# Kernel tuning notes

Measured on AMD Instinct MI355X. Metric: run time of the kernel, lower is better.

## Reference

```python
import jax, jax.numpy as jnp
import numpy as np

N, F, E = 100000, 128, 600000
EPS = 1e-5

def setup_inputs() -> dict:
    key = jax.random.key(0)
    ks = jax.random.split(key, 12)
    d = {
        'feature': jax.random.normal(ks[0], (N, F), jnp.float32),
        'edge_index': jax.random.randint(ks[1], (2, E), 0, N, jnp.int64 if jax.config.jax_enable_x64 else jnp.int32).astype(jnp.int32),
        'edge_weight': jax.random.uniform(ks[2], (E,), jnp.float32),
        'Ws': jax.random.normal(ks[3], (F, F), jnp.float32) * (2.0 / F) ** 0.5,
        'bs': jnp.zeros((F,), jnp.float32),
        'Wi': jax.random.normal(ks[4], (F, F), jnp.float32) * (2.0 / F) ** 0.5,
        'bi': jnp.zeros((F,), jnp.float32),
        'Wr': jax.random.normal(ks[5], (F, F), jnp.float32) * (2.0 / F) ** 0.5,
        'br': jnp.zeros((F,), jnp.float32),
        'gamma': jnp.ones((F,), jnp.float32),
        'beta': jnp.zeros((F,), jnp.float32),
        'WtoI': jax.random.normal(ks[6], (2 * F, F), jnp.float32) * (1.0 / (2 * F)) ** 0.5,
        'btoI': jnp.zeros((F,), jnp.float32),
        'WtoR': jax.random.normal(ks[7], (F, F), jnp.float32) * (1.0 / F) ** 0.5,
        'btoR': jnp.zeros((F,), jnp.float32),
        'Wout': jax.random.normal(ks[8], (3 * F, 3), jnp.float32) * (2.0 / (3 * F)) ** 0.5,
        'bout': jnp.zeros((3,), jnp.float32),
    }
    return d

def _bn(x, gamma, beta):
    # BatchNorm1d in training mode: batch mean, biased variance
    m = x.mean(axis=0)
    v = x.var(axis=0)
    return gamma * (x - m) * jax.lax.rsqrt(v + EPS) + beta

def reference(feature, edge_index, edge_weight, Ws, bs, Wi, bi, Wr, br,
              gamma, beta, WtoI, btoI, WtoR, btoR, Wout, bout):
    n = feature.shape[0]
    s = jax.nn.relu(_bn(feature @ Ws + bs + feature, gamma, beta))
    i = jax.nn.relu(_bn(feature @ Wi + bi + feature, gamma, beta))
    r = jax.nn.relu(_bn(feature @ Wr + br + feature, gamma, beta))
    # message passing: gather i at source nodes, weight, scatter-add to dest
    src, dst = edge_index[0], edge_index[1]
    msg = i[src] * edge_weight[:, None]                      # [E, F]
    neighbor_i = jax.ops.segment_sum(msg, dst, num_segments=n)  # [N, F]
    toI = jnp.concatenate([s, neighbor_i], axis=1) @ WtoI + btoI
    toR = i @ WtoR + btoR
    s1 = s - toI
    i1 = i + toI - toR
    r1 = toR + r
    logits = jnp.concatenate([s1, i1, r1], axis=-1) @ Wout + bout  # [N, 3]
    return jax.nn.softmax(logits, axis=-1)
```

## Files before the change

kernel.cpp:

```cpp
#include <hip/hip_runtime.h>
#include <math.h>

#define NFEAT 128
#define EPSBN 1e-5f
#define LDA 136
#define NREP 8

typedef __attribute__((ext_vector_type(8))) short short8;
typedef __attribute__((ext_vector_type(4))) float f32x4;

__device__ __forceinline__ unsigned short f2bf(float x) {
  union { float f; unsigned u; } v; v.f = x;
  unsigned r = v.u + 0x7FFF + ((v.u >> 16) & 1);
  return (unsigned short)(r >> 16);
}
__device__ __forceinline__ float bf2f(unsigned short h) {
  union { unsigned u; float f; } v; v.u = (unsigned)h << 16;
  return v.f;
}

__global__ __launch_bounds__(256) void kp_params(
    const float* __restrict__ Ws, const float* __restrict__ Wi,
    const float* __restrict__ Wr,
    const float* __restrict__ WtoI, const float* __restrict__ btoI,
    const float* __restrict__ WtoR, const float* __restrict__ btoR,
    const float* __restrict__ Wout, const float* __restrict__ bout,
    short* __restrict__ Whi,
    float* __restrict__ MT, float* __restrict__ cb)
{
  const int tid = threadIdx.x;
  if (blockIdx.x < 24) {
    int t = blockIdx.x * 256 + tid;
    int m   = t >> 11;
    int rem = t & 2047;
    int kf  = rem >> 9;
    int kg  = (rem >> 7) & 3;
    int c   = rem & 127;
    const float* W = (m == 0) ? Ws : ((m == 1) ? Wi : Wr);
    short hb[8];
#pragma unroll
    for (int j = 0; j < 8; j++) {
      int k = kf * 32 + kg * 8 + j;
      float w = W[(size_t)k * NFEAT + c] + (k == c ? 1.0f : 0.0f);
      hb[j] = (short)f2bf(w);
    }
    int base = ((m * 16 + kf * 4 + kg) << 10) + (c << 3);
    *(short8*)&Whi[base] = *(short8*)hb;
    return;
  }

  int t = (blockIdx.x - 24) * 256 + tid;
  int cl = t / 512;
  int idx = t - cl * 512;
  int part = idx >> 7, k = idx & 127;
  float val;
  if (part == 0) {
    float s = Wout[k * 3 + cl];
    for (int f = 0; f < 128; f++)
      s = fmaf(WtoI[k * 128 + f],
               Wout[(128 + f) * 3 + cl] - Wout[f * 3 + cl], s);
    val = s;
  } else if (part == 1) {
    float s = Wout[(128 + k) * 3 + cl];
    for (int f = 0; f < 128; f++)
      s = fmaf(WtoR[k * 128 + f],
               Wout[(256 + f) * 3 + cl] - Wout[(128 + f) * 3 + cl], s);
    val = s;
  } else if (part == 2) {
    val = Wout[(256 + k) * 3 + cl];
  } else {
    float s = 0.f;
    for (int f = 0; f < 128; f++)
      s = fmaf(WtoI[(128 + k) * 128 + f],
               Wout[(128 + f) * 3 + cl] - Wout[f * 3 + cl], s);
    val = s;
  }
  MT[cl * 512 + idx] = val;

  if (blockIdx.x == 24 && tid < 3) {
    float s = bout[tid];
    for (int f = 0; f < 128; f++) {
      s = fmaf(btoI[f], Wout[(128 + f) * 3 + tid] - Wout[f * 3 + tid], s);
      s = fmaf(btoR[f], Wout[(256 + f) * 3 + tid] - Wout[(128 + f) * 3 + tid], s);
    }
    cb[tid] = s;
  }
}

__global__ __launch_bounds__(512, 2) void k1a_store(
    const float* __restrict__ feat,
    const short* __restrict__ Whi,
    const float* __restrict__ bs, const float* __restrict__ bi,
    const float* __restrict__ br,
    float* __restrict__ stats,
    unsigned short* __restrict__ Pb,
    int N, int ntiles)
{
  __shared__ short Ah[2][64 * LDA];

  const int tid  = threadIdx.x;
  const int lane = tid & 63;
  const int wv   = tid >> 6;
  const int colb = wv * 16 + (lane & 15);
  const int kg   = lane >> 4;
  const int krow = kg * 8;

  const int sr = tid >> 3;
  const int so = tid & 7;

  const float bias[3] = {bs[colb], bi[colb], br[colb]};
  float ssum[3] = {0.f, 0.f, 0.f}, ssq[3] = {0.f, 0.f, 0.f};
  const size_t nf = (size_t)N * NFEAT;

  float4 pf[4];
  {
    int gr = blockIdx.x * 64 + sr; if (gr >= N) gr = N - 1;
    const float4* s4 = (const float4*)(feat + (size_t)gr * NFEAT + so * 16);
#pragma unroll
    for (int q = 0; q < 4; q++) pf[q] = s4[q];
    short hbuf[16];
#pragma unroll
    for (int q = 0; q < 4; q++) {
      float xs[4] = {pf[q].x, pf[q].y, pf[q].z, pf[q].w};
#pragma unroll
      for (int cc = 0; cc < 4; cc++) hbuf[q * 4 + cc] = (short)f2bf(xs[cc]);
    }
    *(short8*)&Ah[0][sr * LDA + so * 16]     = *(short8*)(hbuf);
    *(short8*)&Ah[0][sr * LDA + so * 16 + 8] = *(short8*)(hbuf + 8);
  }
  __syncthreads();

  int cur = 0;
  for (int tile = blockIdx.x; tile < ntiles; tile += gridDim.x) {
    const int row0 = tile * 64;
    const int ntile = tile + gridDim.x;
    const bool have_next = ntile < ntiles;

    if (have_next) {
      int gr = ntile * 64 + sr; if (gr >= N) gr = N - 1;
      const float4* s4 = (const float4*)(feat + (size_t)gr * NFEAT + so * 16);
#pragma unroll
      for (int q = 0; q < 4; q++) pf[q] = s4[q];
    }

    const short* ah_c = &Ah[cur][0];

    f32x4 acc[3][4];
#pragma unroll
    for (int m = 0; m < 3; m++)
#pragma unroll
      for (int rf = 0; rf < 4; rf++)
        acc[m][rf] = (f32x4){0.f, 0.f, 0.f, 0.f};

#pragma unroll
    for (int kf = 0; kf < 4; kf++) {
      short8 bh[3];
#pragma unroll
      for (int m = 0; m < 3; m++) {
        int fb = ((m * 16 + kf * 4 + kg) << 10) + (colb << 3);
        bh[m] = *(const short8*)&Whi[fb];
      }
      short8 ah[4];
#pragma unroll
      for (int rf = 0; rf < 4; rf++) {
        int off = (rf * 16 + (lane & 15)) * LDA + kf * 32 + krow;
        ah[rf] = *(const short8*)&ah_c[off];
      }
#pragma unroll
      for (int m = 0; m < 3; m++) {
#pragma unroll
        for (int rf = 0; rf < 4; rf++) {
          acc[m][rf] = __builtin_amdgcn_mfma_f32_16x16x32_bf16(
              ah[rf], bh[m], acc[m][rf], 0, 0, 0);
        }
      }
    }

#pragma unroll
    for (int rf = 0; rf < 4; rf++) {
      int lrb = rf * 16 + kg * 4;
#pragma unroll
      for (int g = 0; g < 4; g++) {
        int gr = row0 + lrb + g;
        bool ok = gr < N;
#pragma unroll
        for (int m = 0; m < 3; m++) {
          float v = acc[m][rf][g] + bias[m];
          if (ok) {
            ssum[m] += v;
            ssq[m]  += v * v;
            Pb[(size_t)m * nf + (size_t)gr * NFEAT + colb] = f2bf(v);
          }
        }
      }
    }

    if (have_next) {
      short hbuf[16];
#pragma unroll
      for (int q = 0; q < 4; q++) {
        float xs[4] = {pf[q].x, pf[q].y, pf[q].z, pf[q].w};
#pragma unroll
        for (int cc = 0; cc < 4; cc++) hbuf[q * 4 + cc] = (short)f2bf(xs[cc]);
      }
      int nb = cur ^ 1;
      *(short8*)&Ah[nb][sr * LDA + so * 16]     = *(short8*)(hbuf);
      *(short8*)&Ah[nb][sr * LDA + so * 16 + 8] = *(short8*)(hbuf + 8);
    }
    asm volatile("s_waitcnt lgkmcnt(0)" ::: "memory");
    __builtin_amdgcn_s_barrier();
    cur ^= 1;
  }

#pragma unroll
  for (int m = 0; m < 3; m++) {
    float s = ssum[m], q = ssq[m];
    s += __shfl_xor(s, 16); s += __shfl_xor(s, 32);
    q += __shfl_xor(q, 16); q += __shfl_xor(q, 32);
    if (kg == 0) {
      unsafeAtomicAdd(&stats[m * 256 + colb], s);
      unsafeAtomicAdd(&stats[m * 256 + 128 + colb], q);
    }
  }
}

__global__ void k_bn(
    const float* __restrict__ stats,
    const float* __restrict__ gamma, const float* __restrict__ beta,
    const float* __restrict__ MT,
    float4* __restrict__ A4, float4* __restrict__ B4, float invN)
{
  int t = threadIdx.x;
  if (t < 384) {
    int m = t >> 7, c = t & 127;
    float mu = stats[m * 256 + c] * invN;
    float var = stats[m * 256 + 128 + c] * invN - mu * mu;
    float a = gamma[c] * rsqrtf(var + EPSBN);
    float kv = beta[c] - mu * a;
    int idx = m * 128 + (c & 7) * 16 + (c >> 3);
    A4[idx] = make_float4(MT[0 * 512 + m * 128 + c],
                          MT[1 * 512 + m * 128 + c],
                          MT[2 * 512 + m * 128 + c], a);
    if (m == 1)
      B4[idx] = make_float4(MT[0 * 512 + 384 + c],
                            MT[1 * 512 + 384 + c],
                            MT[2 * 512 + 384 + c], kv);
    else
      B4[idx] = make_float4(0.f, 0.f, 0.f, kv);
  }
}

__global__ __launch_bounds__(256) void k1g_post(
    const unsigned short* __restrict__ Pb,
    const float4* __restrict__ A4, const float4* __restrict__ B4,
    float* __restrict__ slogA, float* __restrict__ qv,
    float* __restrict__ logit3R, int N, int N4, int nrt)
{
  __shared__ float4 A4s[384];
  __shared__ float4 B4s[384];
  const int tid = threadIdx.x;
  for (int i = tid; i < 384; i += 256) { A4s[i] = A4[i]; B4s[i] = B4[i]; }
  __syncthreads();

  const int l15 = tid & 15;
  const int rg  = tid >> 4;
  const size_t nf = (size_t)N * NFEAT;

  for (int it = blockIdx.x; it < nrt; it += gridDim.x) {
    if (tid < 128) {
      int rep = tid >> 4;
      int zr = it * 16 + (tid & 15);
      if (zr < N)
        *(float4*)&logit3R[(size_t)rep * N4 + (size_t)zr * 4] =
            make_float4(0.f, 0.f, 0.f, 0.f);
    }

    int row = it * 16 + rg;
    if (row >= N) continue;

    float s0 = 0.f, s1 = 0.f, s2 = 0.f;
    float q0 = 0.f, q1 = 0.f, q2 = 0.f;
#pragma unroll
    for (int m = 0; m < 3; m++) {
      const uint4* p4 =
          (const uint4*)(Pb + (size_t)m * nf + (size_t)row * NFEAT + l15 * 8);
      uint4 u = p4[0];
      unsigned dw[4] = {u.x, u.y, u.z, u.w};
#pragma unroll
      for (int d = 0; d < 4; d++) {
        {
          float4 ab = A4s[m * 128 + (2 * d) * 16 + l15];
          float4 bq = B4s[m * 128 + (2 * d) * 16 + l15];
          float P = bf2f((unsigned short)(dw[d] & 0xffffu));
          float v = fmaxf(fmaf(ab.w, P, bq.w), 0.f);
          s0 = fmaf(v, ab.x, s0); s1 = fmaf(v, ab.y, s1); s2 = fmaf(v, ab.z, s2);
          q0 = fmaf(v, bq.x, q0); q1 = fmaf(v, bq.y, q1); q2 = fmaf(v, bq.z, q2);
        }
        {
          float4 ab = A4s[m * 128 + (2 * d + 1) * 16 + l15];
          float4 bq = B4s[m * 128 + (2 * d + 1) * 16 + l15];
          float P = bf2f((unsigned short)(dw[d] >> 16));
          float v = fmaxf(fmaf(ab.w, P, bq.w), 0.f);
          s0 = fmaf(v, ab.x, s0); s1 = fmaf(v, ab.y, s1); s2 = fmaf(v, ab.z, s2);
          q0 = fmaf(v, bq.x, q0); q1 = fmaf(v, bq.y, q1); q2 = fmaf(v, bq.z, q2);
        }
      }
    }
#pragma unroll
    for (int off = 1; off < 16; off <<= 1) {
      s0 += __shfl_xor(s0, off); s1 += __shfl_xor(s1, off);
      s2 += __shfl_xor(s2, off);
      q0 += __shfl_xor(q0, off); q1 += __shfl_xor(q1, off);
      q2 += __shfl_xor(q2, off);
    }
    if (l15 == 0) {
      *(float4*)&slogA[(size_t)row * 4] = make_float4(s0, s1, s2, 0.f);
      *(float4*)&qv[(size_t)row * 4]    = make_float4(q0, q1, q2, 0.f);
    }
  }
}

__global__ __launch_bounds__(256) void k_edge(
    const int* __restrict__ eidx, const float* __restrict__ ew,
    const float* __restrict__ q, float* __restrict__ logit3R,
    int E, int N4)
{
  const int wid  = (blockIdx.x * 256 + threadIdx.x) >> 6;
  const int lane = threadIdx.x & 63;
  const int el   = lane / 3;
  const int comp = lane - el * 3;
  if (el >= 21) return;
  const int e = wid * 21 + el;
  if (e >= E) return;

  int src = eidx[e];
  int dst = eidx[E + e];
  float w = ew[e];
  float qvv = q[(size_t)src * 4 + comp];
  int rep = wid & (NREP - 1);
  unsafeAtomicAdd(&logit3R[(size_t)rep * N4 + (size_t)dst * 4 + comp], qvv * w);
}

__global__ __launch_bounds__(256) void k4_final(
    const float* __restrict__ slogA, const float* __restrict__ logit3R,
    const float* __restrict__ cb,
    float* __restrict__ out, int N, int N4)
{
  int r = blockIdx.x * 256 + threadIdx.x;
  if (r >= N) return;
  float4 S = *(const float4*)&slogA[(size_t)r * 4];
  float l0 = S.x + cb[0], l1 = S.y + cb[1], l2 = S.z + cb[2];
#pragma unroll
  for (int rep = 0; rep < NREP; rep++) {
    float4 L = *(const float4*)&logit3R[(size_t)rep * N4 + (size_t)r * 4];
    l0 += L.x; l1 += L.y; l2 += L.z;
  }
  float mx = fmaxf(l0, fmaxf(l1, l2));
  float e0 = expf(l0 - mx), e1 = expf(l1 - mx), e2 = expf(l2 - mx);
  float inv = 1.f / (e0 + e1 + e2);
  out[(size_t)r * 3 + 0] = e0 * inv;
  out[(size_t)r * 3 + 1] = e1 * inv;
  out[(size_t)r * 3 + 2] = e2 * inv;
}

extern "C" void kernel_launch(void* const* d_in, const int* in_sizes, int n_in,
                              void* d_out, int out_size, void* d_ws, size_t ws_size,
                              hipStream_t stream)
{
  const float* feat  = (const float*)d_in[0];
  const int*   eidx  = (const int*)  d_in[1];
  const float* ew    = (const float*)d_in[2];
  const float* Ws    = (const float*)d_in[3];
  const float* bs    = (const float*)d_in[4];
  const float* Wi    = (const float*)d_in[5];
  const float* bi    = (const float*)d_in[6];
  const float* Wr    = (const float*)d_in[7];
  const float* br    = (const float*)d_in[8];
  const float* gamma = (const float*)d_in[9];
  const float* beta  = (const float*)d_in[10];
  const float* WtoI  = (const float*)d_in[11];
  const float* btoI  = (const float*)d_in[12];
  const float* WtoR  = (const float*)d_in[13];
  const float* btoR  = (const float*)d_in[14];
  const float* Wout  = (const float*)d_in[15];
  const float* bout  = (const float*)d_in[16];

  const int N = in_sizes[0] / NFEAT;
  const int E = in_sizes[2];
  const int N4 = 4 * N;
  const float invN = 1.0f / (float)N;
  float* out = (float*)d_out;

  float* logit3R = (float*)d_ws;
  float* slogA   = logit3R + (size_t)NREP * N4;
  float* qv      = slogA + 4 * (size_t)N;
  float* stats   = qv + 4 * (size_t)N;
  float* MT      = stats + 768;
  float* cb      = MT + 1536;
  float4* A4     = (float4*)(cb + 4);
  float4* B4     = A4 + 384;
  short* Whi     = (short*)(B4 + 384);
  unsigned short* Pb = (unsigned short*)(Whi + 49152);

  hipMemsetAsync(stats, 0, 768 * sizeof(float), stream);

  const int nt = (N + 63) / 64;
  const int g1 = (nt + 2) / 3;
  const int nrt = (N + 15) / 16;

  kp_params<<<30, 256, 0, stream>>>(Ws, Wi, Wr, WtoI, btoI, WtoR, btoR,
                                    Wout, bout, Whi, MT, cb);
  k1a_store<<<g1, 512, 0, stream>>>(feat, Whi, bs, bi, br, stats, Pb, N, nt);
  k_bn<<<1, 384, 0, stream>>>(stats, gamma, beta, MT, A4, B4, invN);
  k1g_post<<<2048, 256, 0, stream>>>(Pb, A4, B4, slogA, qv, logit3R,
                                     N, N4, nrt);
  const int nwaves = (E + 20) / 21;
  k_edge<<<(nwaves + 3) / 4, 256, 0, stream>>>(eidx, ew, qv, logit3R, E, N4);
  k4_final<<<(N + 255) / 256, 256, 0, stream>>>(slogA, logit3R, cb, out, N, N4);
}
```

Before: 126.9 us.

## Replace BN stat atomics with per-block partials and a reduction kernel; retile GEMM

The node GEMM kernel now uses 256-thread blocks over 32-row tiles on a fixed grid of 1536 blocks, and it drops the double-buffered prefetch in favour of a simple load-then-compute loop. Each block writes its BatchNorm sum and sum-of-squares to its own partial buffer instead of issuing float atomics. A small reduction kernel sums the partials, and the BN coefficient computation moves into the post kernel's prologue, so the memset and the separate k_bn launch go away. The aim is to remove atomic contention, a memset and a launch, at the cost of losing the load/compute overlap and adding an extra reduction pass.

```diff
diff --git a/kernel.cpp b/kernel.cpp
--- a/kernel.cpp
+++ b/kernel.cpp
@@ -5,6 +5,7 @@
 #define EPSBN 1e-5f
 #define LDA 136
 #define NREP 8
+#define G1GRID 1536
 
 typedef __attribute__((ext_vector_type(8))) short short8;
 typedef __attribute__((ext_vector_type(4))) float f32x4;
@@ -87,179 +88,163 @@
   }
 }
 
-__global__ __launch_bounds__(512, 2) void k1a_store(
+__global__ __launch_bounds__(256, 4) void k1a_store(
     const float* __restrict__ feat,
     const short* __restrict__ Whi,
     const float* __restrict__ bs, const float* __restrict__ bi,
     const float* __restrict__ br,
-    float* __restrict__ stats,
+    float* __restrict__ Spart,
     unsigned short* __restrict__ Pb,
     int N, int ntiles)
 {
-  __shared__ short Ah[2][64 * LDA];
+  __shared__ short Ah[32 * LDA];
 
   const int tid  = threadIdx.x;
   const int lane = tid & 63;
   const int wv   = tid >> 6;
-  const int colb = wv * 16 + (lane & 15);
+  const int l15  = lane & 15;
   const int kg   = lane >> 4;
   const int krow = kg * 8;
-
-  const int sr = tid >> 3;
-  const int so = tid & 7;
-
-  const float bias[3] = {bs[colb], bi[colb], br[colb]};
-  float ssum[3] = {0.f, 0.f, 0.f}, ssq[3] = {0.f, 0.f, 0.f};
+  const int sr   = tid >> 3;
+  const int so   = tid & 7;
+
+  const int col0 = wv * 32 + l15;
+  const int col1 = wv * 32 + 16 + l15;
+
+  float bias0[3], bias1[3];
+  {
+    const float* Bm[3] = {bs, bi, br};
+#pragma unroll
+    for (int m = 0; m < 3; m++) { bias0[m] = Bm[m][col0]; bias1[m] = Bm[m][col1]; }
+  }
+  float ssum0[3] = {0.f, 0.f, 0.f}, ssq0[3] = {0.f, 0.f, 0.f};
+  float ssum1[3] = {0.f, 0.f, 0.f}, ssq1[3] = {0.f, 0.f, 0.f};
   const size_t nf = (size_t)N * NFEAT;
 
-  float4 pf[4];
-  {
-    int gr = blockIdx.x * 64 + sr; if (gr >= N) gr = N - 1;
-    const float4* s4 = (const float4*)(feat + (size_t)gr * NFEAT + so * 16);
-#pragma unroll
-    for (int q = 0; q < 4; q++) pf[q] = s4[q];
-    short hbuf[16];
-#pragma unroll
-    for (int q = 0; q < 4; q++) {
-      float xs[4] = {pf[q].x, pf[q].y, pf[q].z, pf[q].w};
-#pragma unroll
-      for (int cc = 0; cc < 4; cc++) hbuf[q * 4 + cc] = (short)f2bf(xs[cc]);
-    }
-    *(short8*)&Ah[0][sr * LDA + so * 16]     = *(short8*)(hbuf);
-    *(short8*)&Ah[0][sr * LDA + so * 16 + 8] = *(short8*)(hbuf + 8);
-  }
-  __syncthreads();
-
-  int cur = 0;
   for (int tile = blockIdx.x; tile < ntiles; tile += gridDim.x) {
-    const int row0 = tile * 64;
-    const int ntile = tile + gridDim.x;
-    const bool have_next = ntile < ntiles;
-
-    if (have_next) {
-      int gr = ntile * 64 + sr; if (gr >= N) gr = N - 1;
+    const int row0 = tile * 32;
+    {
+      int gr = row0 + sr; if (gr >= N) gr = N - 1;
       const float4* s4 = (const float4*)(feat + (size_t)gr * NFEAT + so * 16);
-#pragma unroll
-      for (int q = 0; q < 4; q++) pf[q] = s4[q];
-    }
-
-    const short* ah_c = &Ah[cur][0];
-
-    f32x4 acc[3][4];
-#pragma unroll
-    for (int m = 0; m < 3; m++)
-#pragma unroll
-      for (int rf = 0; rf < 4; rf++)
-        acc[m][rf] = (f32x4){0.f, 0.f, 0.f, 0.f};
-
-#pragma unroll
-    for (int kf = 0; kf < 4; kf++) {
-      short8 bh[3];
-#pragma unroll
-      for (int m = 0; m < 3; m++) {
-        int fb = ((m * 16 + kf * 4 + kg) << 10) + (colb << 3);
-        bh[m] = *(const short8*)&Whi[fb];
+      short hbuf[16];
+#pragma unroll
+      for (int q = 0; q < 4; q++) {
+        float4 f = s4[q];
+        float xs[4] = {f.x, f.y, f.z, f.w};
+#pragma unroll
+        for (int cc = 0; cc < 4; cc++) hbuf[q * 4 + cc] = (short)f2bf(xs[cc]);
       }
-      short8 ah[4];
-#pragma unroll
-      for (int rf = 0; rf < 4; rf++) {
-        int off = (rf * 16 + (lane & 15)) * LDA + kf * 32 + krow;
-        ah[rf] = *(const short8*)&ah_c[off];
+      *(short8*)&Ah[sr * LDA + so * 16]     = *(short8*)(hbuf);
+      *(short8*)&Ah[sr * LDA + so * 16 + 8] = *(short8*)(hbuf + 8);
+    }
+    asm volatile("s_waitcnt lgkmcnt(0)" ::: "memory");
+    __builtin_amdgcn_s_barrier();
+
+#pragma unroll
+    for (int m = 0; m < 3; m++) {
+      f32x4 a00 = {0.f,0.f,0.f,0.f}, a01 = {0.f,0.f,0.f,0.f};
+      f32x4 a10 = {0.f,0.f,0.f,0.f}, a11 = {0.f,0.f,0.f,0.f};
+#pragma unroll
+      for (int kf = 0; kf < 4; kf++) {
+        int fb0 = ((m * 16 + kf * 4 + kg) << 10) + (col0 << 3);
+        int fb1 = ((m * 16 + kf * 4 + kg) << 10) + (col1 << 3);
+        short8 b0 = *(const short8*)&Whi[fb0];
+        short8 b1 = *(const short8*)&Whi[fb1];
+        short8 ar0 = *(const short8*)&Ah[(l15) * LDA + kf * 32 + krow];
+        short8 ar1 = *(const short8*)&Ah[(16 + l15) * LDA + kf * 32 + krow];
+        a00 = __builtin_amdgcn_mfma_f32_16x16x32_bf16(ar0, b0, a00, 0, 0, 0);
+        a01 = __builtin_amdgcn_mfma_f32_16x16x32_bf16(ar1, b0, a01, 0, 0, 0);
+        a10 = __builtin_amdgcn_mfma_f32_16x16x32_bf16(ar0, b1, a10, 0, 0, 0);
+        a11 = __builtin_amdgcn_mfma_f32_16x16x32_bf16(ar1, b1, a11, 0, 0, 0);
       }
 #pragma unroll
-      for (int m = 0; m < 3; m++) {
-#pragma unroll
-        for (int rf = 0; rf < 4; rf++) {
-          acc[m][rf] = __builtin_amdgcn_mfma_f32_16x16x32_bf16(
-              ah[rf], bh[m], acc[m][rf], 0, 0, 0);
+      for (int g = 0; g < 4; g++) {
+        int gr0 = row0 + kg * 4 + g;
+        int gr1 = row0 + 16 + kg * 4 + g;
+        if (gr0 < N) {
+          float v = a00[g] + bias0[m];
+          ssum0[m] += v; ssq0[m] += v * v;
+          Pb[(size_t)m * nf + (size_t)gr0 * NFEAT + col0] = f2bf(v);
+          float w = a10[g] + bias1[m];
+          ssum1[m] += w; ssq1[m] += w * w;
+          Pb[(size_t)m * nf + (size_t)gr0 * NFEAT + col1] = f2bf(w);
+        }
+        if (gr1 < N) {
+          float v = a01[g] + bias0[m];
+          ssum0[m] += v; ssq0[m] += v * v;
+          Pb[(size_t)m * nf + (size_t)gr1 * NFEAT + col0] = f2bf(v);
+          float w = a11[g] + bias1[m];
+          ssum1[m] += w; ssq1[m] += w * w;
+          Pb[(size_t)m * nf + (size_t)gr1 * NFEAT + col1] = f2bf(w);
         }
       }
     }
-
-#pragma unroll
-    for (int rf = 0; rf < 4; rf++) {
-      int lrb = rf * 16 + kg * 4;
-#pragma unroll
-      for (int g = 0; g < 4; g++) {
-        int gr = row0 + lrb + g;
-        bool ok = gr < N;
-#pragma unroll
-        for (int m = 0; m < 3; m++) {
-          float v = acc[m][rf][g] + bias[m];
-          if (ok) {
-            ssum[m] += v;
-            ssq[m]  += v * v;
-            Pb[(size_t)m * nf + (size_t)gr * NFEAT + colb] = f2bf(v);
-          }
-        }
-      }
-    }
-
-    if (have_next) {
-      short hbuf[16];
-#pragma unroll
-      for (int q = 0; q < 4; q++) {
-        float xs[4] = {pf[q].x, pf[q].y, pf[q].z, pf[q].w};
-#pragma unroll
-        for (int cc = 0; cc < 4; cc++) hbuf[q * 4 + cc] = (short)f2bf(xs[cc]);
-      }
-      int nb = cur ^ 1;
-      *(short8*)&Ah[nb][sr * LDA + so * 16]     = *(short8*)(hbuf);
-      *(short8*)&Ah[nb][sr * LDA + so * 16 + 8] = *(short8*)(hbuf + 8);
-    }
     asm volatile("s_waitcnt lgkmcnt(0)" ::: "memory");
     __builtin_amdgcn_s_barrier();
-    cur ^= 1;
-  }
-
+  }
+
+  float* sp = Spart + (size_t)blockIdx.x * 768;
 #pragma unroll
   for (int m = 0; m < 3; m++) {
-    float s = ssum[m], q = ssq[m];
-    s += __shfl_xor(s, 16); s += __shfl_xor(s, 32);
-    q += __shfl_xor(q, 16); q += __shfl_xor(q, 32);
+    float s0 = ssum0[m], q0 = ssq0[m], s1 = ssum1[m], q1 = ssq1[m];
+    s0 += __shfl_xor(s0, 16); s0 += __shfl_xor(s0, 32);
+    q0 += __shfl_xor(q0, 16); q0 += __shfl_xor(q0, 32);
+    s1 += __shfl_xor(s1, 16); s1 += __shfl_xor(s1, 32);
+    q1 += __shfl_xor(q1, 16); q1 += __shfl_xor(q1, 32);
     if (kg == 0) {
-      unsafeAtomicAdd(&stats[m * 256 + colb], s);
-      unsafeAtomicAdd(&stats[m * 256 + 128 + colb], q);
-    }
-  }
-}
-
-__global__ void k_bn(
+      sp[m * 256 + col0]       = s0;
+      sp[m * 256 + 128 + col0] = q0;
+      sp[m * 256 + col1]       = s1;
+      sp[m * 256 + 128 + col1] = q1;
+    }
+  }
+}
+
+__global__ __launch_bounds__(256) void k_red(
+    const float* __restrict__ Spart, float* __restrict__ stats)
+{
+  __shared__ float red[256];
+  const int tid = threadIdx.x;
+  const int sidx = blockIdx.x * 64 + (tid & 63);
+  const int chunk = tid >> 6;
+  float s = 0.f;
+  for (int b = chunk * 384; b < chunk * 384 + 384; b++)
+    s += Spart[(size_t)b * 768 + sidx];
+  red[tid] = s;
+  __syncthreads();
+  if (tid < 64)
+    stats[blockIdx.x * 64 + tid] =
+        (red[tid] + red[64 + tid]) + (red[128 + tid] + red[192 + tid]);
+}
+
+__global__ __launch_bounds__(256) void k1g_post(
+    const unsigned short* __restrict__ Pb,
     const float* __restrict__ stats,
     const float* __restrict__ gamma, const float* __restrict__ beta,
     const float* __restrict__ MT,
-    float4* __restrict__ A4, float4* __restrict__ B4, float invN)
-{
-  int t = threadIdx.x;
-  if (t < 384) {
-    int m = t >> 7, c = t & 127;
+    float* __restrict__ slogA, float* __restrict__ qv,
+    float* __restrict__ logit3R, int N, int N4, int nrt, float invN)
+{
+  __shared__ float4 A4s[384];
+  __shared__ float4 B4s[384];
+  const int tid = threadIdx.x;
+  for (int i = tid; i < 384; i += 256) {
+    int m = i >> 7, c = i & 127;
     float mu = stats[m * 256 + c] * invN;
     float var = stats[m * 256 + 128 + c] * invN - mu * mu;
     float a = gamma[c] * rsqrtf(var + EPSBN);
     float kv = beta[c] - mu * a;
     int idx = m * 128 + (c & 7) * 16 + (c >> 3);
-    A4[idx] = make_float4(MT[0 * 512 + m * 128 + c],
-                          MT[1 * 512 + m * 128 + c],
-                          MT[2 * 512 + m * 128 + c], a);
+    A4s[idx] = make_float4(MT[0 * 512 + m * 128 + c],
+                           MT[1 * 512 + m * 128 + c],
+                           MT[2 * 512 + m * 128 + c], a);
     if (m == 1)
-      B4[idx] = make_float4(MT[0 * 512 + 384 + c],
-                            MT[1 * 512 + 384 + c],
-                            MT[2 * 512 + 384 + c], kv);
+      B4s[idx] = make_float4(MT[0 * 512 + 384 + c],
+                             MT[1 * 512 + 384 + c],
+                             MT[2 * 512 + 384 + c], kv);
     else
-      B4[idx] = make_float4(0.f, 0.f, 0.f, kv);
-  }
-}
-
-__global__ __launch_bounds__(256) void k1g_post(
-    const unsigned short* __restrict__ Pb,
-    const float4* __restrict__ A4, const float4* __restrict__ B4,
-    float* __restrict__ slogA, float* __restrict__ qv,
-    float* __restrict__ logit3R, int N, int N4, int nrt)
-{
-  __shared__ float4 A4s[384];
-  __shared__ float4 B4s[384];
-  const int tid = threadIdx.x;
-  for (int i = tid; i < 384; i += 256) { A4s[i] = A4[i]; B4s[i] = B4[i]; }
+      B4s[idx] = make_float4(0.f, 0.f, 0.f, kv);
+  }
   __syncthreads();
 
   const int l15 = tid & 15;
@@ -397,23 +382,20 @@
   float* stats   = qv + 4 * (size_t)N;
   float* MT      = stats + 768;
   float* cb      = MT + 1536;
-  float4* A4     = (float4*)(cb + 4);
-  float4* B4     = A4 + 384;
-  short* Whi     = (short*)(B4 + 384);
+  float* Spart   = cb + 4;
+  short* Whi     = (short*)(Spart + (size_t)G1GRID * 768);
   unsigned short* Pb = (unsigned short*)(Whi + 49152);
 
-  hipMemsetAsync(stats, 0, 768 * sizeof(float), stream);
-
-  const int nt = (N + 63) / 64;
-  const int g1 = (nt + 2) / 3;
-  const int nrt = (N + 15) / 16;
+  const int nt32 = (N + 31) / 32;
+  const int nrt  = (N + 15) / 16;
 
   kp_params<<<30, 256, 0, stream>>>(Ws, Wi, Wr, WtoI, btoI, WtoR, btoR,
                                     Wout, bout, Whi, MT, cb);
-  k1a_store<<<g1, 512, 0, stream>>>(feat, Whi, bs, bi, br, stats, Pb, N, nt);
-  k_bn<<<1, 384, 0, stream>>>(stats, gamma, beta, MT, A4, B4, invN);
-  k1g_post<<<2048, 256, 0, stream>>>(Pb, A4, B4, slogA, qv, logit3R,
-                                     N, N4, nrt);
+  k1a_store<<<G1GRID, 256, 0, stream>>>(feat, Whi, bs, bi, br, Spart, Pb,
+                                        N, nt32);
+  k_red<<<12, 256, 0, stream>>>(Spart, stats);
+  k1g_post<<<2048, 256, 0, stream>>>(Pb, stats, gamma, beta, MT,
+                                     slogA, qv, logit3R, N, N4, nrt, invN);
   const int nwaves = (E + 20) / 21;
   k_edge<<<(nwaves + 3) / 4, 256, 0, stream>>>(eidx, ew, qv, logit3R, E, N4);
   k4_final<<<(N + 255) / 256, 256, 0, stream>>>(slogA, logit3R, cb, out, N, N4);
```

New measurement: 150.1 us. 1.18x slower.
